# Performance work log

Hardware: AMD Instinct MI355X
Metric: run time of the kernel (lower is better)

The kernel has to match this reference:

```python
import jax, jax.numpy as jnp
import numpy as np

DIM = 256
B, W_IN, H_IN = 8, 96, 96


def setup_inputs() -> dict:
    key = jax.random.key(0)
    k1, k2, k3 = jax.random.split(key, 3)
    x = jax.random.normal(k1, (B, W_IN, H_IN, DIM), dtype=jnp.float32)
    # Conv2d(dim, 3*dim, kernel_size=1): weight (3C, C) (1x1 spatial dropped), bias (3C,)
    w_qkv = jax.random.normal(k2, (3 * DIM, DIM), dtype=jnp.float32) * (1.0 / np.sqrt(DIM))
    b_qkv = jax.random.normal(k3, (3 * DIM,), dtype=jnp.float32) * 0.01
    return {"x": x, "w_qkv": w_qkv, "b_qkv": b_qkv}


def reference(x, w_qkv, b_qkv):
    # x: (B, W, H, C) -> transpose(3,1) -> (B, C, H, W)
    xt = jnp.transpose(x, (0, 3, 2, 1))
    # 1x1 conv == channel GEMM
    qvk = jnp.einsum('bchw,oc->bohw', xt, w_qkv) + b_qkv[None, :, None, None]
    q, k, v = jnp.split(qvk, 3, axis=1)  # each (B, C, H, W)
    Bn, C, H, W = q.shape

    q_t = jnp.transpose(q, (0, 2, 1, 3))            # (B, H, C, W)
    qk = q_t.reshape(Bn, H * C, W)                   # (B, H*C, W)
    qf = q_t.reshape(Bn, H, C * W)                   # (B, H, C*W)
    kq = jnp.transpose(k, (0, 1, 3, 2)).reshape(Bn, C * W, H)  # (B, C*W, H)
    ms = jax.nn.softmax(jnp.matmul(qf, kq), axis=-1)  # (B, H, H) attention over H

    kf = jnp.transpose(k, (0, 3, 2, 1)).reshape(Bn, W, H * C)  # (B, W, H*C)
    ma = jax.nn.softmax(jnp.matmul(kf, qk), axis=-1)  # (B, W, W) attention over W

    vq = jnp.transpose(v, (0, 2, 1, 3)).reshape(Bn, H, C * W)  # (B, H, C*W)
    vk = jnp.transpose(v, (0, 3, 2, 1)).reshape(Bn, W, H * C)  # (B, W, H*C)

    ms = jnp.matmul(ms, vq).reshape(Bn, H, C, W)     # view(B, H, C, W)
    ms = jnp.transpose(ms, (0, 2, 1, 3))             # (B, C, H, W)
    ma = jnp.matmul(ma, vk).reshape(Bn, W, H, C)     # view(B, W, H, C)
    ma = jnp.transpose(ma, (0, 3, 2, 1))             # (B, C, H, W)

    # final transpose(3,1): (B, C, H, W) -> (B, W, H, C)
    return jnp.transpose(ms + ma, (0, 3, 2, 1))
```

## Files before the change

kernel.cpp:

```cpp
#include <hip/hip_runtime.h>
#include <math.h>

#define SQ 96
#define CQ 256
#define HWQ 9216
#define PIXQ 73728

typedef __attribute__((ext_vector_type(8))) __bf16 bf16x8;
typedef __attribute__((ext_vector_type(4))) float f32x4;

union FragU { uint4 u; bf16x8 b; };

__device__ inline uint32_t bf16_rne_u(float f) {
  uint32_t u = __float_as_uint(f);
  return (u + 0x7FFFu + ((u >> 16) & 1u)) >> 16;
}
__device__ inline uint32_t pack_split(float f) {
  uint32_t hi = bf16_rne_u(f);
  float rem = f - __uint_as_float(hi << 16);
  uint32_t lo = __float_as_uint(rem) >> 16;
  return hi | (lo << 16);
}

__device__ inline const uint32_t* swzc(const uint32_t* base, int row, int colb) {
  return base + row * 32 + ((colb ^ ((row & 7) << 4)) >> 2);
}

__device__ inline void lds_dma16(const void* g, void* l) {
  __builtin_amdgcn_global_load_lds(
      (const __attribute__((address_space(1))) uint32_t*)g,
      (__attribute__((address_space(3))) uint32_t*)l, 16, 0, 0);
}

__device__ inline void pack8_store(float4 va, float4 vb_, int m, int kc,
                                   int k8, uint32_t* __restrict__ dst) {
  uint32_t p0 = pack_split(va.x), p1 = pack_split(va.y);
  uint32_t p2 = pack_split(va.z), p3 = pack_split(va.w);
  uint32_t p4 = pack_split(vb_.x), p5 = pack_split(vb_.y);
  uint32_t p6 = pack_split(vb_.z), p7 = pack_split(vb_.w);
  uint32_t h[4], l[4];
  h[0] = (p0 & 0xFFFFu) | (p1 << 16);
  h[1] = (p2 & 0xFFFFu) | (p3 << 16);
  h[2] = (p4 & 0xFFFFu) | (p5 << 16);
  h[3] = (p6 & 0xFFFFu) | (p7 << 16);
  l[0] = (p0 >> 16) | (p1 & 0xFFFF0000u);
  l[1] = (p2 >> 16) | (p3 & 0xFFFF0000u);
  l[2] = (p4 >> 16) | (p5 & 0xFFFF0000u);
  l[3] = (p6 >> 16) | (p7 & 0xFFFF0000u);
  int swz = (m & 7) << 4;
  uint32_t* rowp = dst + ((size_t)m * 8 + kc) * 32;
  *(uint4*)(rowp + (((k8 * 16) ^ swz) >> 2)) = *(uint4*)h;
  *(uint4*)(rowp + (((64 + k8 * 16) ^ swz) >> 2)) = *(uint4*)l;
}

__global__ __launch_bounds__(256) void gemm_g_kernel(
    const float* __restrict__ w, float* __restrict__ Gf) {
  const int cp = blockIdx.x;
  const int c = threadIdx.x;
  float acc = 0.0f;
#pragma unroll 4
  for (int o = 0; o < 256; ++o)
    acc += w[o * 256 + c] * w[(256 + o) * 256 + cp];
  Gf[c * 256 + cp] = acc;
}

__global__ __launch_bounds__(256) void prep_vec_kernel(
    const float* __restrict__ w, const float* __restrict__ bias,
    float* __restrict__ tvec, float* __restrict__ svec) {
  const int c = threadIdx.x;
  float t = 0.0f, s = 0.0f;
#pragma unroll 4
  for (int o = 0; o < 256; ++o) {
    t += bias[o] * w[(256 + o) * 256 + c];
    s += bias[256 + o] * w[o * 256 + c];
  }
  tvec[c] = t;
  svec[c] = s;
}

__global__ __launch_bounds__(256) void pack_b_kernel(
    const float* __restrict__ Gf, const float* __restrict__ w,
    uint32_t* __restrict__ Bps) {
  int t = blockIdx.x * 256 + threadIdx.x;
  int e = t * 8;
  int m = e >> 8;
  int rem = e & 255;
  const float* s = (m < 256) ? (Gf + (size_t)m * 256 + rem)
                             : (w + (size_t)(m + 256) * 256 + rem);
  float4 va = *(const float4*)s;
  float4 vb_ = *(const float4*)(s + 4);
  pack8_store(va, vb_, m, rem >> 5, (rem & 31) >> 3, Bps);
}

__global__ __launch_bounds__(256) void split_x_kernel(
    const float* __restrict__ x, const float* __restrict__ tvec,
    const float* __restrict__ svec, uint32_t* __restrict__ xps,
    float* __restrict__ alpha, float* __restrict__ gamma) {
  int t = blockIdx.x * 256 + threadIdx.x;
  int e = t * 8;
  int m = e >> 8;
  int rem = e & 255;
  const float* s = x + (size_t)m * 256 + rem;
  float4 va = *(const float4*)s;
  float4 vb_ = *(const float4*)(s + 4);
  pack8_store(va, vb_, m, rem >> 5, (rem & 31) >> 3, xps);

  const float* tv = tvec + rem;
  const float* sv = svec + rem;
  float td = va.x * tv[0] + va.y * tv[1] + va.z * tv[2] + va.w * tv[3]
           + vb_.x * tv[4] + vb_.y * tv[5] + vb_.z * tv[6] + vb_.w * tv[7];
  float sd = va.x * sv[0] + va.y * sv[1] + va.z * sv[2] + va.w * sv[3]
           + vb_.x * sv[4] + vb_.y * sv[5] + vb_.z * sv[6] + vb_.w * sv[7];
#pragma unroll
  for (int off = 16; off > 0; off >>= 1) {
    td += __shfl_xor(td, off);
    sd += __shfl_xor(sd, off);
  }
  if ((threadIdx.x & 31) == 0) {
    int b = m / HWQ;
    int r = m - b * HWQ;
    int ww = r / SQ;
    int hh = r - ww * SQ;
    atomicAdd(alpha + b * SQ + hh, td);
    atomicAdd(gamma + b * SQ + ww, sd);
  }
}

__global__ __launch_bounds__(256) void qkv_gemm_mfma(
    const uint32_t* __restrict__ xps, const uint32_t* __restrict__ Bps,
    const float* __restrict__ bias, ushort* __restrict__ yps,
    ushort* __restrict__ vb) {
  __shared__ uint32_t Apk[128 * 32];
  __shared__ uint32_t Bpk[128 * 32];
  const int tid = threadIdx.x;
  const int lane = tid & 63;
  const int wid = tid >> 6;
  const int wm = wid >> 1, wn = wid & 1;
  const int lr = lane & 15, quad = lane >> 4;
  const int lin = (blockIdx.x & 7) * 288 + (blockIdx.x >> 3);
  const int m0 = (lin >> 2) * 128, n0 = (lin & 3) * 128;
  const int srow = tid >> 3;
  const int scol = (tid & 7) * 4;

  const uint32_t* aP = xps + (size_t)(m0 + srow) * 256 + scol;
  const uint32_t* bP = Bps + (size_t)(n0 + srow) * 256 + scol;

  f32x4 acc[4][4] = {};

  for (int kc = 0; kc < 8; ++kc) {
#pragma unroll
    for (int j = 0; j < 4; ++j) {
      lds_dma16(aP + j * 8192 + kc * 32, &Apk[j * 1024 + tid * 4]);
      lds_dma16(bP + j * 8192 + kc * 32, &Bpk[j * 1024 + tid * 4]);
    }
    __syncthreads();

    FragU ah[4], al[4], bh[4], bl[4];
#pragma unroll
    for (int t = 0; t < 4; ++t) {
      const int ra = wm * 64 + t * 16 + lr;
      ah[t].u = *(const uint4*)swzc(Apk, ra, quad * 16);
      al[t].u = *(const uint4*)swzc(Apk, ra, 64 + quad * 16);
      const int rb = wn * 64 + t * 16 + lr;
      bh[t].u = *(const uint4*)swzc(Bpk, rb, quad * 16);
      bl[t].u = *(const uint4*)swzc(Bpk, rb, 64 + quad * 16);
    }
#pragma unroll
    for (int i = 0; i < 4; ++i)
#pragma unroll
      for (int j = 0; j < 4; ++j) {
        acc[i][j] = __builtin_amdgcn_mfma_f32_16x16x32_bf16(al[i].b, bh[j].b, acc[i][j], 0, 0, 0);
        acc[i][j] = __builtin_amdgcn_mfma_f32_16x16x32_bf16(ah[i].b, bl[j].b, acc[i][j], 0, 0, 0);
        acc[i][j] = __builtin_amdgcn_mfma_f32_16x16x32_bf16(ah[i].b, bh[j].b, acc[i][j], 0, 0, 0);
      }
    __syncthreads();
  }

  if (n0 < 256) {
#pragma unroll
    for (int i = 0; i < 4; ++i) {
      const int growb = m0 + wm * 64 + i * 16 + quad * 4;
#pragma unroll
      for (int r = 0; r < 4; ++r) {
        int p = growb + r;
        size_t b16 = (size_t)p * 512;
        int sw = (p & 7) << 4;
#pragma unroll
        for (int j = 0; j < 4; ++j) {
          int o = n0 + wn * 64 + j * 16 + lr;
          int ci = o & 31, kc = o >> 5;
          uint32_t ps = pack_split(acc[i][j][r]);
          size_t rb = b16 + (size_t)kc * 64;
          yps[rb + (((ci * 2) ^ sw) >> 1)] = (ushort)ps;
          yps[rb + (((64 + ci * 2) ^ sw) >> 1)] = (ushort)(ps >> 16);
        }
      }
    }
  } else {
#pragma unroll
    for (int i = 0; i < 4; ++i) {
      const int growb = m0 + wm * 64 + i * 16 + quad * 4;
#pragma unroll
      for (int r = 0; r < 4; ++r) {
        int p = growb + r;
        int b = p / HWQ;
        int rem = p - b * HWQ;
        int ww = rem / SQ;
        int hh = rem - ww * SQ;
        size_t opix = (size_t)b * HWQ + (size_t)hh * SQ + ww;
#pragma unroll
        for (int j = 0; j < 4; ++j) {
          int o = n0 + wn * 64 + j * 16 + lr;
          float val = acc[i][j][r] + bias[256 + o];
          vb[opix * 256 + (o - 256)] = (ushort)bf16_rne_u(val);
        }
      }
    }
  }
}

__global__ __launch_bounds__(256) void attn_scores_mfma(
    const ushort* __restrict__ xf, const ushort* __restrict__ yf,
    float* __restrict__ Sp) {
  __shared__ uint32_t Xpk[96 * 32];
  __shared__ uint32_t Ypk[96 * 32];
  const int tid = threadIdx.x;
  const int lane = tid & 63;
  const int wid = tid >> 6;
  const int wm = wid >> 1, wn = wid & 1;
  const int lr = lane & 15, quad = lane >> 4;
  const int chunk = blockIdx.x;
  const int b = blockIdx.y;
  const int which = blockIdx.z;
  const ushort* Xf = which ? yf : xf;
  const ushort* Yf = which ? xf : yf;
  const int srow = tid >> 3;
  const int byteoff = (tid & 7) * 16;

  f32x4 acc[3][3] = {};

  for (int it = 0; it < 24; ++it) {
    int kout = chunk * 3 + (it >> 3);
    int kc = it & 7;
#pragma unroll
    for (int j = 0; j < 3; ++j) {
      int row = j * 32 + srow;
      int pm = which ? (row * SQ + kout) : (kout * SQ + row);
      int pix = b * HWQ + pm;
      int nom = byteoff ^ (((row & 7) ^ (pix & 7)) << 4);
      size_t off = ((size_t)pix * 8 + kc) * 64 + (nom >> 1);
      lds_dma16(Xf + off, &Xpk[j * 1024 + tid * 4]);
      lds_dma16(Yf + off, &Ypk[j * 1024 + tid * 4]);
    }
    __syncthreads();

    FragU xh[3], xl[3], yh[3], yl[3];
#pragma unroll
    for (int t = 0; t < 3; ++t) {
      const int rx = wm * 48 + t * 16 + lr;
      xh[t].u = *(const uint4*)swzc(Xpk, rx, quad * 16);
      xl[t].u = *(const uint4*)swzc(Xpk, rx, 64 + quad * 16);
      const int ry = wn * 48 + t * 16 + lr;
      yh[t].u = *(const uint4*)swzc(Ypk, ry, quad * 16);
      yl[t].u = *(const uint4*)swzc(Ypk, ry, 64 + quad * 16);
    }
#pragma unroll
    for (int i = 0; i < 3; ++i)
#pragma unroll
      for (int j = 0; j < 3; ++j) {
        acc[i][j] = __builtin_amdgcn_mfma_f32_16x16x32_bf16(xl[i].b, yh[j].b, acc[i][j], 0, 0, 0);
        acc[i][j] = __builtin_amdgcn_mfma_f32_16x16x32_bf16(xh[i].b, yl[j].b, acc[i][j], 0, 0, 0);
        acc[i][j] = __builtin_amdgcn_mfma_f32_16x16x32_bf16(xh[i].b, yh[j].b, acc[i][j], 0, 0, 0);
      }
    __syncthreads();
  }
  float* S = Sp + ((size_t)(which * 8 + b) * 32 + chunk) * (size_t)HWQ;
#pragma unroll
  for (int i = 0; i < 3; ++i)
#pragma unroll
    for (int r = 0; r < 4; ++r)
#pragma unroll
      for (int j = 0; j < 3; ++j) {
        int row = wm * 48 + i * 16 + quad * 4 + r;
        int col = wn * 48 + j * 16 + lr;
        S[(size_t)row * SQ + col] = acc[i][j][r];
      }
}

__global__ __launch_bounds__(256) void softmax_p(
    const float* __restrict__ Sp, const float* __restrict__ alpha,
    const float* __restrict__ gamma, ushort* __restrict__ Pms,
    ushort* __restrict__ Pma) {
  const int tid = threadIdx.x;
  const int lane = tid & 63;
  const int row = blockIdx.x * 4 + (tid >> 6);
  const int wsel = row >= 768;
  const int rr = row - wsel * 768;
  const int b = rr / SQ;
  const int hr = rr - b * SQ;
  const float* base = Sp + ((size_t)(wsel * 8 + b) * 32) * (size_t)HWQ
                      + (size_t)hr * SQ;
  float v0 = 0.0f, s1 = 0.0f;
#pragma unroll 4
  for (int ch = 0; ch < 32; ++ch) {
    const float* p = base + (size_t)ch * HWQ;
    v0 += p[lane];
    if (lane < 32) s1 += p[64 + lane];
  }
  const float* corr = (wsel ? gamma : alpha) + b * SQ;
  v0 += corr[lane];
  ushort* q = wsel ? (Pma + (size_t)rr * SQ) : (Pms + (size_t)rr * SQ);
  float v1 = (lane < 32) ? (s1 + corr[64 + lane]) : -3.0e38f;
  float m = fmaxf(v0, v1);
#pragma unroll
  for (int off = 32; off > 0; off >>= 1) m = fmaxf(m, __shfl_xor(m, off));
  float e0 = __expf(v0 - m);
  float e1 = (lane < 32) ? __expf(v1 - m) : 0.0f;
  float s = e0 + e1;
#pragma unroll
  for (int off = 32; off > 0; off >>= 1) s += __shfl_xor(s, off);
  float inv = 1.0f / s;
  q[lane] = (ushort)bf16_rne_u(e0 * inv);
  if (lane < 32) q[64 + lane] = (ushort)bf16_rne_u(e1 * inv);
}

__global__ __launch_bounds__(256) void attn_apply_mfma(
    const ushort* __restrict__ vb, const ushort* __restrict__ P,
    float* __restrict__ out, const int which) {
  __shared__ ushort Vt[256 * 40];
  const int tid = threadIdx.x;
  const int lane = tid & 63;
  const int wid = tid >> 6;
  const int wm = wid >> 1, wn = wid & 1;
  const int lr = lane & 15, quad = lane >> 4;
  const int xi = blockIdx.x;
  const int b = blockIdx.y;

  f32x4 acc[3][8] = {};

  for (int k0 = 0; k0 < 96; k0 += 32) {
#pragma unroll
    for (int j = 0; j < 8; ++j) {
      int bi = j * 256 + tid;
      int c2 = bi & 127;
      int k2 = bi >> 7;
      int k = k0 + k2 * 2;
      int c = c2 * 2;
      size_t r0, r1;
      if (which == 0) {
        r0 = ((size_t)b * HWQ + (size_t)k * SQ + xi) * CQ + c;
        r1 = r0 + (size_t)SQ * CQ;
      } else {
        r0 = ((size_t)b * HWQ + (size_t)xi * SQ + k) * CQ + c;
        r1 = r0 + CQ;
      }
      uint32_t a0 = *(const uint32_t*)(vb + r0);
      uint32_t a1 = *(const uint32_t*)(vb + r1);
      uint32_t w0 = (a0 & 0xFFFFu) | (a1 << 16);
      uint32_t w1 = (a0 >> 16) | (a1 & 0xFFFF0000u);
      *(uint32_t*)&Vt[c * 40 + k2 * 2] = w0;
      *(uint32_t*)&Vt[(c + 1) * 40 + k2 * 2] = w1;
    }
    __syncthreads();
    FragU a[3];
#pragma unroll
    for (int t = 0; t < 3; ++t) {
      int row = wm * 48 + t * 16 + lr;
      const ushort* ps = P + ((size_t)b * SQ + row) * SQ + k0 + quad * 8;
      a[t].u = *(const uint4*)ps;
    }
#pragma unroll
    for (int j = 0; j < 8; ++j) {
      int cb = wn * 128 + j * 16 + lr;
      FragU bf;
      bf.u = *(const uint4*)&Vt[cb * 40 + quad * 8];
#pragma unroll
      for (int i = 0; i < 3; ++i)
        acc[i][j] = __builtin_amdgcn_mfma_f32_16x16x32_bf16(a[i].b, bf.b, acc[i][j], 0, 0, 0);
    }
    __syncthreads();
  }

#pragma unroll
  for (int i = 0; i < 3; ++i) {
#pragma unroll
    for (int r = 0; r < 4; ++r) {
      int mrow = wm * 48 + i * 16 + quad * 4 + r;
      size_t obase;
      if (which == 0) obase = (((size_t)b * SQ + xi) * SQ + mrow) * CQ;
      else            obase = (((size_t)b * SQ + mrow) * SQ + xi) * CQ;
#pragma unroll
      for (int j = 0; j < 8; ++j) {
        int c = wn * 128 + j * 16 + lr;
        if (which == 0) out[obase + c] = acc[i][j][r];
        else            out[obase + c] += acc[i][j][r];
      }
    }
  }
}

extern "C" void kernel_launch(void* const* d_in, const int* in_sizes, int n_in,
                              void* d_out, int out_size, void* d_ws,
                              size_t ws_size, hipStream_t stream) {
  const float* x = (const float*)d_in[0];
  const float* w = (const float*)d_in[1];
  const float* bias = (const float*)d_in[2];
  float* out = (float*)d_out;

  ushort* yps = (ushort*)d_ws;
  ushort* vb  = yps + (size_t)PIXQ * 512;
  ushort* Pms = vb + (size_t)PIXQ * 256;
  ushort* Pma = Pms + PIXQ;
  float*  Sp  = (float*)(Pma + PIXQ);
  uint32_t* Bps = (uint32_t*)(Sp + (size_t)2 * 8 * 32 * HWQ);
  float* Gf   = (float*)(Bps + 512 * 256);
  float* tvec = Gf + 65536;
  float* svec = tvec + 256;
  float* alpha = svec + 256;
  float* gamma = alpha + 768;

  uint32_t* xps = (uint32_t*)d_out;

  hipMemsetAsync(alpha, 0, 2 * 768 * sizeof(float), stream);

  gemm_g_kernel<<<dim3(256), 256, 0, stream>>>(w, Gf);
  prep_vec_kernel<<<dim3(1), 256, 0, stream>>>(w, bias, tvec, svec);
  pack_b_kernel<<<dim3(64), 256, 0, stream>>>(Gf, w, Bps);
  split_x_kernel<<<dim3(9216), 256, 0, stream>>>(x, tvec, svec, xps, alpha, gamma);
  qkv_gemm_mfma<<<dim3(2304), 256, 0, stream>>>(xps, Bps, bias, yps, vb);
  attn_scores_mfma<<<dim3(32, 8, 2), 256, 0, stream>>>((const ushort*)xps, yps, Sp);
  softmax_p<<<dim3(384), 256, 0, stream>>>(Sp, alpha, gamma, Pms, Pma);
  attn_apply_mfma<<<dim3(96, 8), 256, 0, stream>>>(vb, Pms, out, 0);
  attn_apply_mfma<<<dim3(96, 8), 256, 0, stream>>>(vb, Pma, out, 1);
}
```

Measured before the change: 471.8 us.

## Fuse weight-prep kernels and replace atomic alpha/gamma accumulation with two-pass reduction

```diff
diff --git a/kernel.cpp b/kernel.cpp
--- a/kernel.cpp
+++ b/kernel.cpp
@@ -53,76 +53,101 @@
   *(uint4*)(rowp + (((64 + k8 * 16) ^ swz) >> 2)) = *(uint4*)l;
 }
 
-__global__ __launch_bounds__(256) void gemm_g_kernel(
-    const float* __restrict__ w, float* __restrict__ Gf) {
-  const int cp = blockIdx.x;
-  const int c = threadIdx.x;
-  float acc = 0.0f;
-#pragma unroll 4
-  for (int o = 0; o < 256; ++o)
-    acc += w[o * 256 + c] * w[(256 + o) * 256 + cp];
-  Gf[c * 256 + cp] = acc;
+__global__ __launch_bounds__(256) void prep_b_kernel(
+    const float* __restrict__ w, uint32_t* __restrict__ Bps) {
+  __shared__ float grow[256];
+  const int blk = blockIdx.x;
+  if (blk < 256) {
+    const int cp = threadIdx.x;
+    float acc = 0.0f;
+#pragma unroll 4
+    for (int o = 0; o < 256; ++o)
+      acc += w[o * 256 + blk] * w[(256 + o) * 256 + cp];
+    grow[cp] = acc;
+    __syncthreads();
+    if (threadIdx.x < 32) {
+      int rem = threadIdx.x * 8;
+      float4 va = *(const float4*)(grow + rem);
+      float4 vb_ = *(const float4*)(grow + rem + 4);
+      pack8_store(va, vb_, blk, rem >> 5, (rem & 31) >> 3, Bps);
+    }
+  } else {
+    int r = (blk - 256) * 8 + (threadIdx.x >> 5);
+    int rem = (threadIdx.x & 31) * 8;
+    const float* s = w + (size_t)(512 + r) * 256 + rem;
+    float4 va = *(const float4*)s;
+    float4 vb_ = *(const float4*)(s + 4);
+    pack8_store(va, vb_, 256 + r, rem >> 5, (rem & 31) >> 3, Bps);
+  }
 }
 
 __global__ __launch_bounds__(256) void prep_vec_kernel(
     const float* __restrict__ w, const float* __restrict__ bias,
     float* __restrict__ tvec, float* __restrict__ svec) {
   const int c = threadIdx.x;
-  float t = 0.0f, s = 0.0f;
-#pragma unroll 4
-  for (int o = 0; o < 256; ++o) {
-    t += bias[o] * w[(256 + o) * 256 + c];
-    s += bias[256 + o] * w[o * 256 + c];
-  }
-  tvec[c] = t;
-  svec[c] = s;
-}
-
-__global__ __launch_bounds__(256) void pack_b_kernel(
-    const float* __restrict__ Gf, const float* __restrict__ w,
-    uint32_t* __restrict__ Bps) {
-  int t = blockIdx.x * 256 + threadIdx.x;
-  int e = t * 8;
-  int m = e >> 8;
-  int rem = e & 255;
-  const float* s = (m < 256) ? (Gf + (size_t)m * 256 + rem)
-                             : (w + (size_t)(m + 256) * 256 + rem);
-  float4 va = *(const float4*)s;
-  float4 vb_ = *(const float4*)(s + 4);
-  pack8_store(va, vb_, m, rem >> 5, (rem & 31) >> 3, Bps);
+  if (blockIdx.x == 0) {
+    float t = 0.0f;
+#pragma unroll 4
+    for (int o = 0; o < 256; ++o) t += bias[o] * w[(256 + o) * 256 + c];
+    tvec[c] = t;
+  } else {
+    float s = 0.0f;
+#pragma unroll 4
+    for (int o = 0; o < 256; ++o) s += bias[256 + o] * w[o * 256 + c];
+    svec[c] = s;
+  }
 }
 
 __global__ __launch_bounds__(256) void split_x_kernel(
     const float* __restrict__ x, const float* __restrict__ tvec,
     const float* __restrict__ svec, uint32_t* __restrict__ xps,
+    float* __restrict__ dtp, float* __restrict__ dsp) {
+  int rec = blockIdx.x * 256 + threadIdx.x;
+  int m = rec >> 3;
+  int kc = rec & 7;
+  const float* s = x + (size_t)m * 256 + kc * 32;
+  const float* tv = tvec + kc * 32;
+  const float* sv = svec + kc * 32;
+  float dt = 0.0f, ds = 0.0f;
+#pragma unroll
+  for (int g = 0; g < 4; ++g) {
+    float4 va = *(const float4*)(s + g * 8);
+    float4 vb_ = *(const float4*)(s + g * 8 + 4);
+    pack8_store(va, vb_, m, kc, g, xps);
+    const float* tg = tv + g * 8;
+    const float* sg = sv + g * 8;
+    dt += va.x * tg[0] + va.y * tg[1] + va.z * tg[2] + va.w * tg[3]
+        + vb_.x * tg[4] + vb_.y * tg[5] + vb_.z * tg[6] + vb_.w * tg[7];
+    ds += va.x * sg[0] + va.y * sg[1] + va.z * sg[2] + va.w * sg[3]
+        + vb_.x * sg[4] + vb_.y * sg[5] + vb_.z * sg[6] + vb_.w * sg[7];
+  }
+#pragma unroll
+  for (int off = 1; off < 8; off <<= 1) {
+    dt += __shfl_xor(dt, off);
+    ds += __shfl_xor(ds, off);
+  }
+  if ((rec & 7) == 0) {
+    dtp[m] = dt;
+    dsp[m] = ds;
+  }
+}
+
+__global__ __launch_bounds__(256) void reduce_ag_kernel(
+    const float* __restrict__ dtp, const float* __restrict__ dsp,
     float* __restrict__ alpha, float* __restrict__ gamma) {
-  int t = blockIdx.x * 256 + threadIdx.x;
-  int e = t * 8;
-  int m = e >> 8;
-  int rem = e & 255;
-  const float* s = x + (size_t)m * 256 + rem;
-  float4 va = *(const float4*)s;
-  float4 vb_ = *(const float4*)(s + 4);
-  pack8_store(va, vb_, m, rem >> 5, (rem & 31) >> 3, xps);
-
-  const float* tv = tvec + rem;
-  const float* sv = svec + rem;
-  float td = va.x * tv[0] + va.y * tv[1] + va.z * tv[2] + va.w * tv[3]
-           + vb_.x * tv[4] + vb_.y * tv[5] + vb_.z * tv[6] + vb_.w * tv[7];
-  float sd = va.x * sv[0] + va.y * sv[1] + va.z * sv[2] + va.w * sv[3]
-           + vb_.x * sv[4] + vb_.y * sv[5] + vb_.z * sv[6] + vb_.w * sv[7];
-#pragma unroll
-  for (int off = 16; off > 0; off >>= 1) {
-    td += __shfl_xor(td, off);
-    sd += __shfl_xor(sd, off);
-  }
-  if ((threadIdx.x & 31) == 0) {
-    int b = m / HWQ;
-    int r = m - b * HWQ;
-    int ww = r / SQ;
-    int hh = r - ww * SQ;
-    atomicAdd(alpha + b * SQ + hh, td);
-    atomicAdd(gamma + b * SQ + ww, sd);
+  const int b = blockIdx.x;
+  const int t = threadIdx.x;
+  if (t < 96) {
+    float a = 0.0f;
+#pragma unroll 4
+    for (int wi = 0; wi < 96; ++wi) a += dtp[b * HWQ + wi * SQ + t];
+    alpha[b * SQ + t] = a;
+  } else if (t >= 128 && t < 224) {
+    int wi = t - 128;
+    float g = 0.0f;
+#pragma unroll 4
+    for (int hh = 0; hh < 96; ++hh) g += dsp[b * HWQ + wi * SQ + hh];
+    gamma[b * SQ + wi] = g;
   }
 }
 
@@ -413,20 +438,19 @@
   ushort* Pma = Pms + PIXQ;
   float*  Sp  = (float*)(Pma + PIXQ);
   uint32_t* Bps = (uint32_t*)(Sp + (size_t)2 * 8 * 32 * HWQ);
-  float* Gf   = (float*)(Bps + 512 * 256);
-  float* tvec = Gf + 65536;
+  float* tvec = (float*)(Bps + 512 * 256);
   float* svec = tvec + 256;
   float* alpha = svec + 256;
   float* gamma = alpha + 768;
+  float* dtp = gamma + 768;
+  float* dsp = dtp + PIXQ;
 
   uint32_t* xps = (uint32_t*)d_out;
 
-  hipMemsetAsync(alpha, 0, 2 * 768 * sizeof(float), stream);
-
-  gemm_g_kernel<<<dim3(256), 256, 0, stream>>>(w, Gf);
-  prep_vec_kernel<<<dim3(1), 256, 0, stream>>>(w, bias, tvec, svec);
-  pack_b_kernel<<<dim3(64), 256, 0, stream>>>(Gf, w, Bps);
-  split_x_kernel<<<dim3(9216), 256, 0, stream>>>(x, tvec, svec, xps, alpha, gamma);
+  prep_b_kernel<<<dim3(288), 256, 0, stream>>>(w, Bps);
+  prep_vec_kernel<<<dim3(2), 256, 0, stream>>>(w, bias, tvec, svec);
+  split_x_kernel<<<dim3(2304), 256, 0, stream>>>(x, tvec, svec, xps, dtp, dsp);
+  reduce_ag_kernel<<<dim3(8), 256, 0, stream>>>(dtp, dsp, alpha, gamma);
   qkv_gemm_mfma<<<dim3(2304), 256, 0, stream>>>(xps, Bps, bias, yps, vb);
   attn_scores_mfma<<<dim3(32, 8, 2), 256, 0, stream>>>((const ushort*)xps, yps, Sp);
   softmax_p<<<dim3(384), 256, 0, stream>>>(Sp, alpha, gamma, Pms, Pma);
```

Measured after the change: 436.5 us. 1.08x faster.
